# Kernel optimization log

Hardware: AMD Instinct MI355X
Metric: run time of the kernel (lower is better)

## Reference

```python
import jax, jax.numpy as jnp
import numpy as np

ALPHA = 10.0   # args.alpha softmax sharpness
EPS = 1e-8     # torch CosineSimilarity eps


def setup_inputs() -> dict:
    key = jax.random.key(0)
    k0, k1, k2, k3 = jax.random.split(key, 4)
    B, S, F, D, C = 8, 1024, 32, 128, 16
    Hs = jax.random.normal(k0, (B, S, F, D), dtype=jnp.float32)
    Cj = jax.random.normal(k1, (C, D), dtype=jnp.float32)
    W = jax.random.normal(k2, (D, D), dtype=jnp.float32) * 0.05  # nn.Linear weight [out,in]
    b = jnp.zeros((D,), dtype=jnp.float32)
    importance = jax.random.uniform(k3, (B, S, F), dtype=jnp.float32)
    return {"Hs": Hs, "Cj": Cj, "W": W, "b": b, "importance": importance}


def reference(Hs, Cj, W, b, importance):
    # Hs: [B,S,F,D] features; Cj: [C,D] cluster centers; importance: [B,S,F]
    # Faithful to Model_DTSSOCC.assignment (importance is not None branch),
    # but avoids materializing the broadcasted [B,S,F,C,D] repeat tensors.
    Hn = Hs / jnp.maximum(jnp.linalg.norm(Hs, axis=-1, keepdims=True), EPS)
    Cn = Cj / jnp.maximum(jnp.linalg.norm(Cj, axis=-1, keepdims=True), EPS)
    cos = jnp.einsum('bsfd,cd->bsfc', Hn, Cn)            # cosine_sim4 over dim D
    logits = -ALPHA * 0.5 * (1.0 - cos)                  # -alpha * dists, [B,S,F,C]
    w3 = jax.nn.softmax(logits, axis=3)                  # softmax over centers
    w = jax.nn.softmax(logits, axis=2)                   # softmax over feas
    w3 = jnp.swapaxes(w3, 2, 3)                          # [B,S,C,F]
    w = jnp.swapaxes(w, 2, 3)                            # [B,S,C,F]
    F_tj = jax.nn.relu(jnp.einsum('bsfd,ed->bsfe', Hs, W) + b)  # relu(Linear(F_t))
    # importance update: bmm(w3, importance) then softmax over centers
    imp = jax.nn.softmax(jnp.einsum('bscf,bsf->bsc', w3, importance), axis=2)
    # weighted feature aggregation: bmm(w, F_tj) -> [B,S,C,D]
    f_t_new = jnp.einsum('bscf,bsfd->bscd', w, F_tj)
    return f_t_new, imp
```

## Files before the change

kernel.cpp:

```cpp
#include <hip/hip_runtime.h>
#include <hip/hip_bf16.h>
#include <math.h>

constexpr int Bn = 8, Sn = 1024, Fn = 32, Dn = 128, Cc = 16;
constexpr int NSITE = Bn * Sn;

#define EPSV 1e-8f

typedef __attribute__((ext_vector_type(8))) short bf16x8;
typedef __attribute__((ext_vector_type(4))) short bf16x4;
typedef __attribute__((ext_vector_type(4))) float f32x4;

__device__ inline short f2bf(float x) {
    __hip_bfloat16 h = __float2bfloat16(x);
    short s;
    __builtin_memcpy(&s, &h, sizeof(s));
    return s;
}

__device__ inline bf16x8 cvt8(f32x4 x0, f32x4 x1) {
    bf16x8 r;
    r[0] = f2bf(x0[0]); r[1] = f2bf(x0[1]); r[2] = f2bf(x0[2]); r[3] = f2bf(x0[3]);
    r[4] = f2bf(x1[0]); r[5] = f2bf(x1[1]); r[6] = f2bf(x1[2]); r[7] = f2bf(x1[3]);
    return r;
}

template<int CTRL>
__device__ __forceinline__ float dpp_add(float v) {
    union { float f; int i; } u, r;
    u.f = v;
    r.i = __builtin_amdgcn_update_dpp(0, u.i, CTRL, 0xf, 0xf, true);
    return v + r.f;
}
__device__ __forceinline__ float rowsum16(float v) {
    v = dpp_add<0x121>(v);
    v = dpp_add<0x122>(v);
    v = dpp_add<0x124>(v);
    v = dpp_add<0x128>(v);
    return v;
}
__device__ __forceinline__ float fastrcp(float x) { return __builtin_amdgcn_rcpf(x); }

__global__ void prep_kernel(const float* __restrict__ Cj,
                            const float* __restrict__ W,
                            short* __restrict__ CnPack,
                            short* __restrict__ Wb) {
    const int tid = threadIdx.x;
    if (blockIdx.x < 64) {
        int t = blockIdx.x * 256 + tid;
        int n = t >> 7, k = t & 127;
        short v = f2bf(W[n * Dn + k]);
        int frag = (n >> 4) * 4 + (k >> 5);
        int lane = ((k >> 3) & 3) * 16 + (n & 15);
        Wb[(frag * 64 + lane) * 8 + (k & 7)] = v;
    } else {
        int c = blockIdx.x - 64;
        __shared__ float part[2];
        float v = 0.f, sq = 0.f;
        if (tid < 128) {
            v = Cj[c * Dn + tid];
            sq = v * v;
            #pragma unroll
            for (int off = 32; off > 0; off >>= 1) sq += __shfl_down(sq, off);
        }
        if (tid < 128 && (tid & 63) == 0) part[tid >> 6] = sq;
        __syncthreads();
        if (tid < 128) {
            float cn = v / fmaxf(sqrtf(part[0] + part[1]), EPSV);
            int kt = tid >> 5, ln = ((tid >> 3) & 3) * 16 + c, j = tid & 7;
            CnPack[(kt * 64 + ln) * 8 + j] = f2bf(cn);
        }
    }
}

__launch_bounds__(64, 4)
__global__ void site_kernel(const float* __restrict__ Hs,
                            const short* __restrict__ CnPack,
                            const short* __restrict__ Wb,
                            const float* __restrict__ bvec,
                            const float* __restrict__ imp_in,
                            float* __restrict__ f_out,
                            float* __restrict__ imp_out) {
    __shared__ __align__(16) short F_tjT[128][40];

    const int lane = threadIdx.x;
    const int c16  = lane & 15;
    const int g    = lane >> 4;
    const int site = blockIdx.x;

    const float* hsrc = Hs + (size_t)site * (Fn * Dn);
    const f32x4 zro = {0.f, 0.f, 0.f, 0.f};

    f32x4 x[16];
    #pragma unroll
    for (int kt = 0; kt < 4; ++kt) {
        const f32x4* p0 = (const f32x4*)(hsrc + c16 * Dn + kt * 32 + g * 8);
        const f32x4* p1 = (const f32x4*)(hsrc + (16 + c16) * Dn + kt * 32 + g * 8);
        x[4 * kt + 0] = p0[0];
        x[4 * kt + 1] = p0[1];
        x[4 * kt + 2] = p1[0];
        x[4 * kt + 3] = p1[1];
    }
    bf16x8 bcf[4];
    #pragma unroll
    for (int kt = 0; kt < 4; ++kt)
        bcf[kt] = *(const bf16x8*)&CnPack[(kt * 64 + lane) * 8];
    const float* impp = imp_in + (size_t)site * Fn;
    f32x4 impv0 = *(const f32x4*)(impp + 4 * g);
    f32x4 impv1 = *(const f32x4*)(impp + 16 + 4 * g);

    bf16x8 aF[2][4];
    #pragma unroll
    for (int kt = 0; kt < 4; ++kt) {
        aF[0][kt] = cvt8(x[4 * kt + 0], x[4 * kt + 1]);
        aF[1][kt] = cvt8(x[4 * kt + 2], x[4 * kt + 3]);
    }

    f32x4 gm0 = zro, gm1 = zro, cos0 = zro, cos1 = zro;
    #pragma unroll
    for (int kt = 0; kt < 4; ++kt) {
        gm0  = __builtin_amdgcn_mfma_f32_16x16x32_bf16(aF[0][kt], aF[0][kt], gm0, 0, 0, 0);
        gm1  = __builtin_amdgcn_mfma_f32_16x16x32_bf16(aF[1][kt], aF[1][kt], gm1, 0, 0, 0);
        cos0 = __builtin_amdgcn_mfma_f32_16x16x32_bf16(aF[0][kt], bcf[kt], cos0, 0, 0, 0);
        cos1 = __builtin_amdgcn_mfma_f32_16x16x32_bf16(aF[1][kt], bcf[kt], cos1, 0, 0, 0);
    }

    float e0[4], e1[4];
    #pragma unroll
    for (int r = 0; r < 4; ++r) {
        float q0 = __shfl(gm0[r], 20 * g + r);
        float q1 = __shfl(gm1[r], 20 * g + r);
        float i0 = fastrcp(fmaxf(sqrtf(q0), EPSV));
        float i1 = fastrcp(fmaxf(sqrtf(q1), EPSV));
        e0[r] = __expf(5.0f * cos0[r] * i0);
        e1[r] = __expf(5.0f * cos1[r] * i1);
    }

    bf16x8 wB;
    {
        float sum = 0.f;
        #pragma unroll
        for (int r = 0; r < 4; ++r) sum += e0[r] + e1[r];
        sum += __shfl_xor(sum, 16);
        sum += __shfl_xor(sum, 32);
        float inv = fastrcp(sum);
        const int srcA = c16 + 16 * ((2 * g) & 3);
        const int srcB = c16 + 16 * ((2 * g + 1) & 3);
        const bool hi = (g >= 2);
        #pragma unroll
        for (int r = 0; r < 4; ++r) {
            float a0 = __shfl(e0[r] * inv, srcA);
            float a1 = __shfl(e1[r] * inv, srcA);
            wB[r] = f2bf(hi ? a1 : a0);
            float b0 = __shfl(e0[r] * inv, srcB);
            float b1 = __shfl(e1[r] * inv, srcB);
            wB[4 + r] = f2bf(hi ? b1 : b0);
        }
    }

    {
        float t = 0.f;
        #pragma unroll
        for (int h = 0; h < 2; ++h) {
            #pragma unroll
            for (int r = 0; r < 4; ++r) {
                float e = h ? e1[r] : e0[r];
                float q3 = rowsum16(e);
                t += e * fastrcp(q3) * (h ? impv1[r] : impv0[r]);
            }
        }
        t += __shfl_xor(t, 16);
        t += __shfl_xor(t, 32);
        float ei = __expf(t);
        float si = rowsum16(ei);
        if (g == 0) imp_out[(size_t)site * Cc + c16] = ei * fastrcp(si);
    }

    #pragma unroll
    for (int nt = 0; nt < 8; ++nt) {
        bf16x8 bw0 = *(const bf16x8*)&Wb[((nt * 4) + 0) * 512 + lane * 8];
        bf16x8 bw1 = *(const bf16x8*)&Wb[((nt * 4) + 1) * 512 + lane * 8];
        bf16x8 bw2 = *(const bf16x8*)&Wb[((nt * 4) + 2) * 512 + lane * 8];
        bf16x8 bw3 = *(const bf16x8*)&Wb[((nt * 4) + 3) * 512 + lane * 8];
        f32x4 acc0 = zro, acc1 = zro;
        acc0 = __builtin_amdgcn_mfma_f32_16x16x32_bf16(aF[0][0], bw0, acc0, 0, 0, 0);
        acc1 = __builtin_amdgcn_mfma_f32_16x16x32_bf16(aF[1][0], bw0, acc1, 0, 0, 0);
        acc0 = __builtin_amdgcn_mfma_f32_16x16x32_bf16(aF[0][1], bw1, acc0, 0, 0, 0);
        acc1 = __builtin_amdgcn_mfma_f32_16x16x32_bf16(aF[1][1], bw1, acc1, 0, 0, 0);
        acc0 = __builtin_amdgcn_mfma_f32_16x16x32_bf16(aF[0][2], bw2, acc0, 0, 0, 0);
        acc1 = __builtin_amdgcn_mfma_f32_16x16x32_bf16(aF[1][2], bw2, acc1, 0, 0, 0);
        acc0 = __builtin_amdgcn_mfma_f32_16x16x32_bf16(aF[0][3], bw3, acc0, 0, 0, 0);
        acc1 = __builtin_amdgcn_mfma_f32_16x16x32_bf16(aF[1][3], bw3, acc1, 0, 0, 0);
        float bb = bvec[nt * 16 + c16];
        bf16x4 p0, p1;
        #pragma unroll
        for (int r = 0; r < 4; ++r) {
            p0[r] = f2bf(fmaxf(acc0[r] + bb, 0.f));
            p1[r] = f2bf(fmaxf(acc1[r] + bb, 0.f));
        }
        *(bf16x4*)&F_tjT[nt * 16 + c16][4 * g]      = p0;
        *(bf16x4*)&F_tjT[nt * 16 + c16][16 + 4 * g] = p1;
    }

    {
        float* op = f_out + (size_t)site * (Cc * Dn);
        #pragma unroll
        for (int nt = 0; nt < 8; ++nt) {
            bf16x8 aFt = *(const bf16x8*)&F_tjT[nt * 16 + c16][8 * g];
            f32x4 o = __builtin_amdgcn_mfma_f32_16x16x32_bf16(aFt, wB, zro, 0, 0, 0);
            *(f32x4*)(op + c16 * Dn + nt * 16 + 4 * g) = o;
        }
    }
}

extern "C" void kernel_launch(void* const* d_in, const int* in_sizes, int n_in,
                              void* d_out, int out_size, void* d_ws, size_t ws_size,
                              hipStream_t stream) {
    const float* Hs  = (const float*)d_in[0];
    const float* Cj  = (const float*)d_in[1];
    const float* W   = (const float*)d_in[2];
    const float* b   = (const float*)d_in[3];
    const float* imp = (const float*)d_in[4];

    float* f_out   = (float*)d_out;
    float* imp_out = f_out + (size_t)NSITE * Cc * Dn;

    short* CnPack = (short*)d_ws;
    short* Wb     = CnPack + Cc * Dn;

    hipLaunchKernelGGL(prep_kernel, dim3(80), dim3(256), 0, stream, Cj, W, CnPack, Wb);
    hipLaunchKernelGGL(site_kernel, dim3(NSITE), dim3(64), 0, stream,
                       Hs, CnPack, Wb, b, imp, f_out, imp_out);
}
```

Before: 46.06 us.

## Process two sites per wavefront to reuse W fragments and shrink LDS

Each 64-thread block now handles two sites, so every W fragment loaded is fed to MFMAs for both sites, halving the W load traffic per site. The ReLU-linear output no longer goes through a full 128x40 LDS buffer. Each 16-column tile is written to a small double-buffered LDS slice and consumed right away by the aggregation MFMA. The trade is higher register pressure from holding two sites' bf16 activations, plus half as many blocks to hide latency.

```diff
diff --git a/kernel.cpp b/kernel.cpp
--- a/kernel.cpp
+++ b/kernel.cpp
@@ -81,134 +81,153 @@
                             const float* __restrict__ imp_in,
                             float* __restrict__ f_out,
                             float* __restrict__ imp_out) {
-    __shared__ __align__(16) short F_tjT[128][40];
+    __shared__ __align__(16) short Ft[2][2][16][40];
 
     const int lane = threadIdx.x;
     const int c16  = lane & 15;
     const int g    = lane >> 4;
-    const int site = blockIdx.x;
-
-    const float* hsrc = Hs + (size_t)site * (Fn * Dn);
+    const int sA   = blockIdx.x * 2;
+    const int sB   = sA + 1;
+
     const f32x4 zro = {0.f, 0.f, 0.f, 0.f};
 
-    f32x4 x[16];
+    bf16x8 aFA[2][4], aFB[2][4];
+    bf16x8 wBA, wBB;
+
     #pragma unroll
-    for (int kt = 0; kt < 4; ++kt) {
-        const f32x4* p0 = (const f32x4*)(hsrc + c16 * Dn + kt * 32 + g * 8);
-        const f32x4* p1 = (const f32x4*)(hsrc + (16 + c16) * Dn + kt * 32 + g * 8);
-        x[4 * kt + 0] = p0[0];
-        x[4 * kt + 1] = p0[1];
-        x[4 * kt + 2] = p1[0];
-        x[4 * kt + 3] = p1[1];
-    }
-    bf16x8 bcf[4];
-    #pragma unroll
-    for (int kt = 0; kt < 4; ++kt)
-        bcf[kt] = *(const bf16x8*)&CnPack[(kt * 64 + lane) * 8];
-    const float* impp = imp_in + (size_t)site * Fn;
-    f32x4 impv0 = *(const f32x4*)(impp + 4 * g);
-    f32x4 impv1 = *(const f32x4*)(impp + 16 + 4 * g);
-
-    bf16x8 aF[2][4];
-    #pragma unroll
-    for (int kt = 0; kt < 4; ++kt) {
-        aF[0][kt] = cvt8(x[4 * kt + 0], x[4 * kt + 1]);
-        aF[1][kt] = cvt8(x[4 * kt + 2], x[4 * kt + 3]);
-    }
-
-    f32x4 gm0 = zro, gm1 = zro, cos0 = zro, cos1 = zro;
-    #pragma unroll
-    for (int kt = 0; kt < 4; ++kt) {
-        gm0  = __builtin_amdgcn_mfma_f32_16x16x32_bf16(aF[0][kt], aF[0][kt], gm0, 0, 0, 0);
-        gm1  = __builtin_amdgcn_mfma_f32_16x16x32_bf16(aF[1][kt], aF[1][kt], gm1, 0, 0, 0);
-        cos0 = __builtin_amdgcn_mfma_f32_16x16x32_bf16(aF[0][kt], bcf[kt], cos0, 0, 0, 0);
-        cos1 = __builtin_amdgcn_mfma_f32_16x16x32_bf16(aF[1][kt], bcf[kt], cos1, 0, 0, 0);
-    }
-
-    float e0[4], e1[4];
-    #pragma unroll
-    for (int r = 0; r < 4; ++r) {
-        float q0 = __shfl(gm0[r], 20 * g + r);
-        float q1 = __shfl(gm1[r], 20 * g + r);
-        float i0 = fastrcp(fmaxf(sqrtf(q0), EPSV));
-        float i1 = fastrcp(fmaxf(sqrtf(q1), EPSV));
-        e0[r] = __expf(5.0f * cos0[r] * i0);
-        e1[r] = __expf(5.0f * cos1[r] * i1);
-    }
-
-    bf16x8 wB;
-    {
-        float sum = 0.f;
+    for (int sp = 0; sp < 2; ++sp) {
+        const int site = sp ? sB : sA;
+        bf16x8 (&aF)[2][4] = sp ? aFB : aFA;
+
+        {
+            f32x4 x[16];
+            const float* hsrc = Hs + (size_t)site * (Fn * Dn);
+            #pragma unroll
+            for (int kt = 0; kt < 4; ++kt) {
+                const f32x4* p0 = (const f32x4*)(hsrc + c16 * Dn + kt * 32 + g * 8);
+                const f32x4* p1 = (const f32x4*)(hsrc + (16 + c16) * Dn + kt * 32 + g * 8);
+                x[4 * kt + 0] = p0[0];
+                x[4 * kt + 1] = p0[1];
+                x[4 * kt + 2] = p1[0];
+                x[4 * kt + 3] = p1[1];
+            }
+            #pragma unroll
+            for (int kt = 0; kt < 4; ++kt) {
+                aF[0][kt] = cvt8(x[4 * kt + 0], x[4 * kt + 1]);
+                aF[1][kt] = cvt8(x[4 * kt + 2], x[4 * kt + 3]);
+            }
+        }
+
+        f32x4 gm0 = zro, gm1 = zro, cos0 = zro, cos1 = zro;
         #pragma unroll
-        for (int r = 0; r < 4; ++r) sum += e0[r] + e1[r];
-        sum += __shfl_xor(sum, 16);
-        sum += __shfl_xor(sum, 32);
-        float inv = fastrcp(sum);
-        const int srcA = c16 + 16 * ((2 * g) & 3);
-        const int srcB = c16 + 16 * ((2 * g + 1) & 3);
-        const bool hi = (g >= 2);
+        for (int kt = 0; kt < 4; ++kt) {
+            bf16x8 bc = *(const bf16x8*)&CnPack[(kt * 64 + lane) * 8];
+            gm0  = __builtin_amdgcn_mfma_f32_16x16x32_bf16(aF[0][kt], aF[0][kt], gm0, 0, 0, 0);
+            gm1  = __builtin_amdgcn_mfma_f32_16x16x32_bf16(aF[1][kt], aF[1][kt], gm1, 0, 0, 0);
+            cos0 = __builtin_amdgcn_mfma_f32_16x16x32_bf16(aF[0][kt], bc, cos0, 0, 0, 0);
+            cos1 = __builtin_amdgcn_mfma_f32_16x16x32_bf16(aF[1][kt], bc, cos1, 0, 0, 0);
+        }
+
+        float e0[4], e1[4];
         #pragma unroll
         for (int r = 0; r < 4; ++r) {
-            float a0 = __shfl(e0[r] * inv, srcA);
-            float a1 = __shfl(e1[r] * inv, srcA);
-            wB[r] = f2bf(hi ? a1 : a0);
-            float b0 = __shfl(e0[r] * inv, srcB);
-            float b1 = __shfl(e1[r] * inv, srcB);
-            wB[4 + r] = f2bf(hi ? b1 : b0);
+            float q0 = __shfl(gm0[r], 20 * g + r);
+            float q1 = __shfl(gm1[r], 20 * g + r);
+            float i0 = fastrcp(fmaxf(sqrtf(q0), EPSV));
+            float i1 = fastrcp(fmaxf(sqrtf(q1), EPSV));
+            e0[r] = __expf(5.0f * cos0[r] * i0);
+            e1[r] = __expf(5.0f * cos1[r] * i1);
+        }
+
+        {
+            float sum = 0.f;
+            #pragma unroll
+            for (int r = 0; r < 4; ++r) sum += e0[r] + e1[r];
+            sum += __shfl_xor(sum, 16);
+            sum += __shfl_xor(sum, 32);
+            float inv = fastrcp(sum);
+            const int srcA = c16 + 16 * ((2 * g) & 3);
+            const int srcB = c16 + 16 * ((2 * g + 1) & 3);
+            const bool hi = (g >= 2);
+            bf16x8 wB;
+            #pragma unroll
+            for (int r = 0; r < 4; ++r) {
+                float a0 = __shfl(e0[r] * inv, srcA);
+                float a1 = __shfl(e1[r] * inv, srcA);
+                wB[r] = f2bf(hi ? a1 : a0);
+                float b0 = __shfl(e0[r] * inv, srcB);
+                float b1 = __shfl(e1[r] * inv, srcB);
+                wB[4 + r] = f2bf(hi ? b1 : b0);
+            }
+            if (sp) wBB = wB; else wBA = wB;
+        }
+
+        {
+            const float* impp = imp_in + (size_t)site * Fn;
+            f32x4 impv0 = *(const f32x4*)(impp + 4 * g);
+            f32x4 impv1 = *(const f32x4*)(impp + 16 + 4 * g);
+            float t = 0.f;
+            #pragma unroll
+            for (int h = 0; h < 2; ++h) {
+                #pragma unroll
+                for (int r = 0; r < 4; ++r) {
+                    float e = h ? e1[r] : e0[r];
+                    float q3 = rowsum16(e);
+                    t += e * fastrcp(q3) * (h ? impv1[r] : impv0[r]);
+                }
+            }
+            t += __shfl_xor(t, 16);
+            t += __shfl_xor(t, 32);
+            float ei = __expf(t);
+            float si = rowsum16(ei);
+            if (g == 0) imp_out[(size_t)site * Cc + c16] = ei * fastrcp(si);
         }
     }
 
-    {
-        float t = 0.f;
-        #pragma unroll
-        for (int h = 0; h < 2; ++h) {
-            #pragma unroll
-            for (int r = 0; r < 4; ++r) {
-                float e = h ? e1[r] : e0[r];
-                float q3 = rowsum16(e);
-                t += e * fastrcp(q3) * (h ? impv1[r] : impv0[r]);
-            }
-        }
-        t += __shfl_xor(t, 16);
-        t += __shfl_xor(t, 32);
-        float ei = __expf(t);
-        float si = rowsum16(ei);
-        if (g == 0) imp_out[(size_t)site * Cc + c16] = ei * fastrcp(si);
-    }
-
+    float* opA = f_out + (size_t)sA * (Cc * Dn);
+    float* opB = f_out + (size_t)sB * (Cc * Dn);
     #pragma unroll
     for (int nt = 0; nt < 8; ++nt) {
-        bf16x8 bw0 = *(const bf16x8*)&Wb[((nt * 4) + 0) * 512 + lane * 8];
-        bf16x8 bw1 = *(const bf16x8*)&Wb[((nt * 4) + 1) * 512 + lane * 8];
-        bf16x8 bw2 = *(const bf16x8*)&Wb[((nt * 4) + 2) * 512 + lane * 8];
-        bf16x8 bw3 = *(const bf16x8*)&Wb[((nt * 4) + 3) * 512 + lane * 8];
-        f32x4 acc0 = zro, acc1 = zro;
-        acc0 = __builtin_amdgcn_mfma_f32_16x16x32_bf16(aF[0][0], bw0, acc0, 0, 0, 0);
-        acc1 = __builtin_amdgcn_mfma_f32_16x16x32_bf16(aF[1][0], bw0, acc1, 0, 0, 0);
-        acc0 = __builtin_amdgcn_mfma_f32_16x16x32_bf16(aF[0][1], bw1, acc0, 0, 0, 0);
-        acc1 = __builtin_amdgcn_mfma_f32_16x16x32_bf16(aF[1][1], bw1, acc1, 0, 0, 0);
-        acc0 = __builtin_amdgcn_mfma_f32_16x16x32_bf16(aF[0][2], bw2, acc0, 0, 0, 0);
-        acc1 = __builtin_amdgcn_mfma_f32_16x16x32_bf16(aF[1][2], bw2, acc1, 0, 0, 0);
-        acc0 = __builtin_amdgcn_mfma_f32_16x16x32_bf16(aF[0][3], bw3, acc0, 0, 0, 0);
-        acc1 = __builtin_amdgcn_mfma_f32_16x16x32_bf16(aF[1][3], bw3, acc1, 0, 0, 0);
+        f32x4 aA0 = zro, aA1 = zro, aB0 = zro, aB1 = zro;
+        #pragma unroll
+        for (int kp = 0; kp < 2; ++kp) {
+            bf16x8 bw0 = *(const bf16x8*)&Wb[((nt * 4) + 2 * kp + 0) * 512 + lane * 8];
+            bf16x8 bw1 = *(const bf16x8*)&Wb[((nt * 4) + 2 * kp + 1) * 512 + lane * 8];
+            aA0 = __builtin_amdgcn_mfma_f32_16x16x32_bf16(aFA[0][2 * kp + 0], bw0, aA0, 0, 0, 0);
+            aA1 = __builtin_amdgcn_mfma_f32_16x16x32_bf16(aFA[1][2 * kp + 0], bw0, aA1, 0, 0, 0);
+            aB0 = __builtin_amdgcn_mfma_f32_16x16x32_bf16(aFB[0][2 * kp + 0], bw0, aB0, 0, 0, 0);
+            aB1 = __builtin_amdgcn_mfma_f32_16x16x32_bf16(aFB[1][2 * kp + 0], bw0, aB1, 0, 0, 0);
+            aA0 = __builtin_amdgcn_mfma_f32_16x16x32_bf16(aFA[0][2 * kp + 1], bw1, aA0, 0, 0, 0);
+            aA1 = __builtin_amdgcn_mfma_f32_16x16x32_bf16(aFA[1][2 * kp + 1], bw1, aA1, 0, 0, 0);
+            aB0 = __builtin_amdgcn_mfma_f32_16x16x32_bf16(aFB[0][2 * kp + 1], bw1, aB0, 0, 0, 0);
+            aB1 = __builtin_amdgcn_mfma_f32_16x16x32_bf16(aFB[1][2 * kp + 1], bw1, aB1, 0, 0, 0);
+        }
         float bb = bvec[nt * 16 + c16];
-        bf16x4 p0, p1;
-        #pragma unroll
-        for (int r = 0; r < 4; ++r) {
-            p0[r] = f2bf(fmaxf(acc0[r] + bb, 0.f));
-            p1[r] = f2bf(fmaxf(acc1[r] + bb, 0.f));
-        }
-        *(bf16x4*)&F_tjT[nt * 16 + c16][4 * g]      = p0;
-        *(bf16x4*)&F_tjT[nt * 16 + c16][16 + 4 * g] = p1;
-    }
-
-    {
-        float* op = f_out + (size_t)site * (Cc * Dn);
-        #pragma unroll
-        for (int nt = 0; nt < 8; ++nt) {
-            bf16x8 aFt = *(const bf16x8*)&F_tjT[nt * 16 + c16][8 * g];
-            f32x4 o = __builtin_amdgcn_mfma_f32_16x16x32_bf16(aFt, wB, zro, 0, 0, 0);
-            *(f32x4*)(op + c16 * Dn + nt * 16 + 4 * g) = o;
+        {
+            bf16x4 p0, p1;
+            #pragma unroll
+            for (int r = 0; r < 4; ++r) {
+                p0[r] = f2bf(fmaxf(aA0[r] + bb, 0.f));
+                p1[r] = f2bf(fmaxf(aA1[r] + bb, 0.f));
+            }
+            *(bf16x4*)&Ft[0][nt & 1][c16][4 * g]      = p0;
+            *(bf16x4*)&Ft[0][nt & 1][c16][16 + 4 * g] = p1;
+            bf16x8 aFt = *(const bf16x8*)&Ft[0][nt & 1][c16][8 * g];
+            f32x4 o = __builtin_amdgcn_mfma_f32_16x16x32_bf16(aFt, wBA, zro, 0, 0, 0);
+            *(f32x4*)(opA + c16 * Dn + nt * 16 + 4 * g) = o;
+        }
+        {
+            bf16x4 p0, p1;
+            #pragma unroll
+            for (int r = 0; r < 4; ++r) {
+                p0[r] = f2bf(fmaxf(aB0[r] + bb, 0.f));
+                p1[r] = f2bf(fmaxf(aB1[r] + bb, 0.f));
+            }
+            *(bf16x4*)&Ft[1][nt & 1][c16][4 * g]      = p0;
+            *(bf16x4*)&Ft[1][nt & 1][c16][16 + 4 * g] = p1;
+            bf16x8 aFt = *(const bf16x8*)&Ft[1][nt & 1][c16][8 * g];
+            f32x4 o = __builtin_amdgcn_mfma_f32_16x16x32_bf16(aFt, wBB, zro, 0, 0, 0);
+            *(f32x4*)(opB + c16 * Dn + nt * 16 + 4 * g) = o;
         }
     }
 }
@@ -229,6 +248,6 @@
     short* Wb     = CnPack + Cc * Dn;
 
     hipLaunchKernelGGL(prep_kernel, dim3(80), dim3(256), 0, stream, Cj, W, CnPack, Wb);
-    hipLaunchKernelGGL(site_kernel, dim3(NSITE), dim3(64), 0, stream,
+    hipLaunchKernelGGL(site_kernel, dim3(NSITE / 2), dim3(64), 0, stream,
                        Hs, CnPack, Wb, b, imp, f_out, imp_out);
 }
```

After: 46.35 us. About the same (+0.6%).
